# Optimization experiments

Measured on AMD Instinct MI355X. Metric: run time of the kernel, lower is better.

## Reference

```python
import jax, jax.numpy as jnp
import numpy as np

B, P, C = 256, 196, 512       # batch, num_pixels, encoder_dim
D, A, E = 512, 256, 256       # decoder_dim, attention_dim, embedding_dim
V, TC = 193, 256              # vocab, caption length (decode steps = TC-1)


def _lin(k, out_d, in_d):
    s = 1.0 / np.sqrt(in_d)
    return jax.random.uniform(k, (out_d, in_d), jnp.float32, -s, s)


def setup_inputs() -> dict:
    key = jax.random.key(0)
    ks = jax.random.split(key, 16)
    lens = jax.random.randint(ks[1], (B,), 2, TC + 1).at[0].set(TC)
    inp = {
        "encoder_output": jax.random.normal(ks[0], (B, P, C), jnp.float32),
        "encoded_captions": jax.random.randint(ks[2], (B, TC), 0, V),
        "caption_lengths": lens[:, None],
        # attention
        "W_enc_att": _lin(ks[3], A, C), "b_enc_att": jnp.zeros((A,), jnp.float32),
        "W_dec_att": _lin(ks[4], A, D), "b_dec_att": jnp.zeros((A,), jnp.float32),
        "W_full_att": _lin(ks[5], 1, A), "b_full_att": jnp.zeros((1,), jnp.float32),
        # embedding (init uniform(-0.1, 0.1) as in init_weigths)
        "embedding": jax.random.uniform(ks[6], (V, E), jnp.float32, -0.1, 0.1),
        # output projection
        "W_fc": jax.random.uniform(ks[7], (V, D), jnp.float32, -0.1, 0.1),
        "b_fc": jnp.zeros((V,), jnp.float32),
        # LSTMCell: input is [emb ; attended_enc] -> E + C
        "W_ih": _lin(ks[8], 4 * D, E + C), "b_ih": jnp.zeros((4 * D,), jnp.float32),
        "W_hh": _lin(ks[9], 4 * D, D), "b_hh": jnp.zeros((4 * D,), jnp.float32),
        # hidden/cell init + gate
        "W_init_h": _lin(ks[10], D, C), "b_init_h": jnp.zeros((D,), jnp.float32),
        "W_init_c": _lin(ks[11], D, C), "b_init_c": jnp.zeros((D,), jnp.float32),
        "W_fbeta": _lin(ks[12], D, C), "b_fbeta": jnp.zeros((D,), jnp.float32),
    }
    return inp


def reference(encoder_output, encoded_captions, caption_lengths,
              W_enc_att, b_enc_att, W_dec_att, b_dec_att, W_full_att, b_full_att,
              embedding, W_fc, b_fc, W_ih, b_ih, W_hh, b_hh,
              W_init_h, b_init_h, W_init_c, b_init_c, W_fbeta, b_fbeta):
    b = encoder_output.shape[0]
    enc = encoder_output.reshape(b, -1, encoder_output.shape[-1])  # [B,P,C]
    lens = caption_lengths[:, 0]
    sort_index = jnp.argsort(-lens)                 # descending length sort
    lens = lens[sort_index]
    enc = enc[sort_index]
    caps = encoded_captions[sort_index]
    decode_lengths = lens - 1
    T = caps.shape[1] - 1                           # static max decode steps

    embs = embedding[caps]                          # [B,TC,E]
    mean_enc = enc.mean(axis=1)                     # [B,C]
    h0 = mean_enc @ W_init_h.T + b_init_h
    c0 = mean_enc @ W_init_c.T + b_init_c

    enc_att = enc @ W_enc_att.T + b_enc_att         # [B,P,A] precomputed
    wf, bf = W_full_att[0], b_full_att[0]

    def step(carry, xs):
        h, c = carry
        emb_t, t = xs
        # soft attention
        dec_att = h @ W_dec_att.T + b_dec_att                       # [B,A]
        scores = jnp.einsum('bpa,a->bp',
                            jax.nn.relu(enc_att + dec_att[:, None, :]), wf) + bf
        alpha = jax.nn.softmax(scores, axis=1)                      # [B,P]
        awe = jnp.einsum('bpc,bp->bc', enc, alpha)                  # [B,C]
        gate = jax.nn.sigmoid(h @ W_fbeta.T + b_fbeta)              # [B,D]
        awe = gate * awe
        # LSTM cell (torch gate order: i,f,g,o); dropout is identity in eval
        x = jnp.concatenate([emb_t, awe], axis=1)                   # [B,E+C]
        gates = x @ W_ih.T + b_ih + h @ W_hh.T + b_hh
        i_g, f_g, g_g, o_g = jnp.split(gates, 4, axis=1)
        c_new = jax.nn.sigmoid(f_g) * c + jax.nn.sigmoid(i_g) * jnp.tanh(g_g)
        h_new = jax.nn.sigmoid(o_g) * jnp.tanh(c_new)
        # shrinking-batch semantics: inactive rows keep state, emit zeros
        active = (t < decode_lengths)[:, None]
        h2 = jnp.where(active, h_new, h)
        c2 = jnp.where(active, c_new, c)
        preds = jnp.where(active, h_new @ W_fc.T + b_fc, 0.0)
        alpha = jnp.where(active, alpha, 0.0)
        return (h2, c2), (preds, alpha)

    xs = (jnp.swapaxes(embs[:, :T], 0, 1), jnp.arange(T))
    _, (preds, alphas) = jax.lax.scan(step, (h0, c0), xs)
    predictions = jnp.swapaxes(preds, 0, 1)   # [B,T,V]
    alphas = jnp.swapaxes(alphas, 0, 1)       # [B,T,P]
    return predictions, caps, decode_lengths, alphas, sort_index
```

## Files before the change

### kernel.cpp

```cpp
#include <hip/hip_runtime.h>
#include <cstdint>
#include <cstddef>


typedef unsigned short u16;
typedef unsigned int u32;
typedef unsigned long long ull;
typedef __attribute__((ext_vector_type(8))) short short8;
typedef __attribute__((ext_vector_type(4))) float f32x4;

__device__ __forceinline__ float sigf(float x){ return 1.f/(1.f+expf(-x)); }
__device__ __forceinline__ u16 f2bf(float f){
  u32 u = __builtin_bit_cast(u32, f);
  u32 r = (u + 0x7fffu + ((u>>16)&1u)) >> 16;
  return (u16)r;
}
__device__ __forceinline__ float bf2f(u16 u){
  u32 x = ((u32)u) << 16;
  return __builtin_bit_cast(float, x);
}

__device__ __forceinline__ void st_dev_f32(float* p, float v){
  __hip_atomic_store(p, v, __ATOMIC_RELAXED, __HIP_MEMORY_SCOPE_AGENT);
}
__device__ __forceinline__ float ld_dev_f32(const float* p){
  return __hip_atomic_load(p, __ATOMIC_RELAXED, __HIP_MEMORY_SCOPE_AGENT);
}
__device__ __forceinline__ void st_dev_u16(u16* p, u16 v){
  __hip_atomic_store(p, v, __ATOMIC_RELAXED, __HIP_MEMORY_SCOPE_AGENT);
}
__device__ __forceinline__ void st_dev_u32(u32* p, u32 v){
  __hip_atomic_store(p, v, __ATOMIC_RELAXED, __HIP_MEMORY_SCOPE_AGENT);
}
__device__ __forceinline__ u32 ld_dev_u32(const u32* p){
  return __hip_atomic_load(p, __ATOMIC_RELAXED, __HIP_MEMORY_SCOPE_AGENT);
}
__device__ __forceinline__ ull ld_dev_u64(const ull* p){
  return __hip_atomic_load(p, __ATOMIC_RELAXED, __HIP_MEMORY_SCOPE_AGENT);
}

__device__ __forceinline__ void flag_store(int* f, int v){
  __syncthreads();
  if (threadIdx.x == 0)
    __hip_atomic_store(f, v, __ATOMIC_RELAXED, __HIP_MEMORY_SCOPE_AGENT);
}
__device__ __forceinline__ void flags_wait(const int* f, int n, int target){
  if (threadIdx.x < 64){
    const int lane = threadIdx.x;
    int spins = 0;
    for (;;){
      int v = (lane < n) ? __hip_atomic_load(&f[lane], __ATOMIC_RELAXED, __HIP_MEMORY_SCOPE_AGENT)
                         : 0x7fffffff;
      if (__all(v >= target)) break;
      if (++spins > (1<<20)) break;
      __builtin_amdgcn_s_sleep(2);
    }
  }
  __syncthreads();
}

__global__ void k_zero(float* a, int na4, float* b, int nb4, int* ctr){
  int i = blockIdx.x*blockDim.x + threadIdx.x;
  int stride = gridDim.x*blockDim.x;
  float4 z = make_float4(0.f,0.f,0.f,0.f);
  for (int j = i; j < na4; j += stride) ((float4*)a)[j] = z;
  for (int j = i; j < nb4; j += stride) ((float4*)b)[j] = z;
  if (i < 512) ctr[i] = 0;
}

__global__ void k_sort(const int* cap_lens, int* si, int* dlw, float* out_dl, float* out_si){
  __shared__ int lens[256];
  int tid = threadIdx.x;
  lens[tid] = cap_lens[tid];
  __syncthreads();
  int L = lens[tid];
  int rank = 0;
  for (int j = 0; j < 256; ++j){
    int Lj = lens[j];
    rank += ((Lj > L) || (Lj == L && j < tid)) ? 1 : 0;
  }
  si[rank] = tid;
  dlw[rank] = L - 1;
  out_dl[rank] = (float)(L - 1);
  out_si[rank] = (float)tid;
}

__global__ void k_caps(const int* caps, const int* si, int* caps_s, float* out_caps){
  int b = blockIdx.x, t = threadIdx.x;
  int v = caps[si[b]*256 + t];
  caps_s[b*256 + t] = v;
  out_caps[b*256 + t] = (float)v;
}

__global__ void k_prep(const float* enc, const int* si, u16* enc_sb){
  int b = blockIdx.x, tid = threadIdx.x;
  const float* src = enc + (size_t)si[b]*100352;
  u16* dst = enc_sb + (size_t)b*100352;
  for (int i = tid; i < 25088; i += 256){
    float4 v = *(const float4*)&src[i*4];
    ushort4 o;
    o.x = f2bf(v.x); o.y = f2bf(v.y); o.z = f2bf(v.z); o.w = f2bf(v.w);
    *(ushort4*)&dst[i*4] = o;
  }
}

__global__ void k_mean(const float* enc, const int* si, u16* mean_bf){
  int b = blockIdx.x, tid = threadIdx.x;
  const float* eb = enc + (size_t)si[b]*100352;
  int cc = 2*tid;
  float s0 = 0.f, s1 = 0.f;
  #pragma unroll 4
  for (int pp = 0; pp < 196; ++pp){
    float2 v = *(const float2*)&eb[(size_t)pp*512 + cc];
    s0 += v.x; s1 += v.y;
  }
  mean_bf[b*512 + cc]     = f2bf(s0 * (1.f/196.f));
  mean_bf[b*512 + cc + 1] = f2bf(s1 * (1.f/196.f));
}

struct ConcatP {
  const float *Wdec,*bdec,*Wfb,*bfb,*Wfc,*bfc,*Wih,*bih,*Whh,*bhh,*Winh,*binh,*Winc,*binc,*Wenc,*emb;
  u16 *Wc0,*Wc1,*Wc3,*Wenc_bf,*emb_bf;
  float *bc0,*bc1,*bc3;
};
__global__ void k_concat(ConcatP p){
  int idx = blockIdx.x*blockDim.x + threadIdx.x;
  int stride = gridDim.x*blockDim.x;
  for (int i = idx; i < 1024*512; i += stride){
    int n = i >> 9, k = i & 511;
    float v = (n < 512) ? p.Winh[n*512 + k] : p.Winc[(n-512)*512 + k];
    p.Wc0[i] = f2bf(v);
  }
  for (int i = idx; i < 1024; i += stride)
    p.bc0[i] = (i < 512) ? p.binh[i] : p.binc[i-512];
  for (int i = idx; i < 1024*512; i += stride){
    int n = i >> 9, k = i & 511;
    float v = (n < 256) ? p.Wdec[n*512+k]
            : (n < 768) ? p.Wfb[(n-256)*512+k]
            : (n < 961) ? p.Wfc[(n-768)*512+k] : 0.f;
    p.Wc1[i] = f2bf(v);
  }
  for (int i = idx; i < 1024; i += stride)
    p.bc1[i] = (i < 256) ? p.bdec[i] : (i < 768) ? p.bfb[i-256] : (i < 961) ? p.bfc[i-768] : 0.f;
  for (int i = idx; i < 2048*1280; i += stride){
    int n = i / 1280, k = i - n*1280;
    int j = n >> 2, g = n & 3, orow = g*512 + j;
    float v = (k < 768) ? p.Wih[orow*768 + k] : p.Whh[orow*512 + (k - 768)];
    p.Wc3[i] = f2bf(v);
  }
  for (int i = idx; i < 2048; i += stride){
    int j = i >> 2, g = i & 3, orow = g*512 + j;
    p.bc3[i] = p.bih[orow] + p.bhh[orow];
  }
  for (int i = idx; i < 256*512; i += stride) p.Wenc_bf[i] = f2bf(p.Wenc[i]);
  for (int i = idx; i < 193*256; i += stride) p.emb_bf[i] = f2bf(p.emb[i]);
}

struct MfmaP {
  const u16* A; const u16* Bw; const float* bias;
  int K, N;
  u16* out_bf;
  u16* h_bf; float* c;
};

template<int MODE, int NT>
__global__ __launch_bounds__(256) void k_mfma(MfmaP p){
  __shared__ __align__(16) unsigned char smem[16384 + 16384*NT];
  u16* As0 = (u16*)smem;
  u16* Bs0 = (u16*)(smem + 16384);

  const int tid  = threadIdx.x;
  const int bn0  = blockIdx.x * 64 * NT;
  const int bm0  = blockIdx.y * 64;
  const int wave = tid >> 6;
  const int lane = tid & 63;
  const int ln   = lane & 15;
  const int quad = lane >> 4;

  f32x4 acc[4][NT] = {};
  short8 pa[2], pb[2*NT];

  const int srow = tid >> 3;
  const int sgc  = tid & 7;

  #pragma unroll
  for (int r = 0; r < 2; ++r)
    pa[r] = *(const short8*)(p.A + (size_t)(bm0 + srow + 32*r)*p.K + sgc*8);
  #pragma unroll
  for (int r = 0; r < 2*NT; ++r)
    pb[r] = *(const short8*)(p.Bw + (size_t)(bn0 + srow + 32*r)*p.K + sgc*8);
  #pragma unroll
  for (int r = 0; r < 2; ++r){
    int row = srow + 32*r;
    *(short8*)&As0[row*64 + ((sgc ^ (row & 7))<<3)] = pa[r];
  }
  #pragma unroll
  for (int r = 0; r < 2*NT; ++r){
    int row = srow + 32*r;
    *(short8*)&Bs0[row*64 + ((sgc ^ (row & 7))<<3)] = pb[r];
  }

  const int nIter = p.K >> 6;
  int ib = 0;
  for (int it = 0; ; ){
    __syncthreads();
    const bool more = (it + 1 < nIter);
    if (more){
      int k0 = (it + 1) << 6;
      #pragma unroll
      for (int r = 0; r < 2; ++r)
        pa[r] = *(const short8*)(p.A + (size_t)(bm0 + srow + 32*r)*p.K + k0 + sgc*8);
      #pragma unroll
      for (int r = 0; r < 2*NT; ++r)
        pb[r] = *(const short8*)(p.Bw + (size_t)(bn0 + srow + 32*r)*p.K + k0 + sgc*8);
    }
    const u16* As = &As0[ib*4096];
    const u16* Bs = &Bs0[ib*4096*NT];
    #pragma unroll
    for (int kk = 0; kk < 2; ++kk){
      short8 af[4], bfr[NT];
      #pragma unroll
      for (int mt = 0; mt < 4; ++mt){
        int row = mt*16 + ln;
        int g = kk*4 + quad;
        af[mt] = *(const short8*)&As[row*64 + ((g ^ (row & 7))<<3)];
      }
      #pragma unroll
      for (int nt = 0; nt < NT; ++nt){
        int row = (wave*NT + nt)*16 + ln;
        int g = kk*4 + quad;
        bfr[nt] = *(const short8*)&Bs[row*64 + ((g ^ (row & 7))<<3)];
      }
      #pragma unroll
      for (int mt = 0; mt < 4; ++mt)
        #pragma unroll
        for (int nt = 0; nt < NT; ++nt)
          acc[mt][nt] = __builtin_amdgcn_mfma_f32_16x16x32_bf16(af[mt], bfr[nt], acc[mt][nt], 0, 0, 0);
    }
    if (!more) break;
    ib ^= 1;
    u16* Aw = &As0[ib*4096];
    u16* Bww = &Bs0[ib*4096*NT];
    #pragma unroll
    for (int r = 0; r < 2; ++r){
      int row = srow + 32*r;
      *(short8*)&Aw[row*64 + ((sgc ^ (row & 7))<<3)] = pa[r];
    }
    #pragma unroll
    for (int r = 0; r < 2*NT; ++r){
      int row = srow + 32*r;
      *(short8*)&Bww[row*64 + ((sgc ^ (row & 7))<<3)] = pb[r];
    }
    ++it;
  }

  #pragma unroll
  for (int nt = 0; nt < NT; ++nt){
    int n = bn0 + (wave*NT + nt)*16 + ln;
    float bv = p.bias[n];
    #pragma unroll
    for (int mt = 0; mt < 4; ++mt)
      #pragma unroll
      for (int r = 0; r < 4; ++r){
        int m = bm0 + mt*16 + quad*4 + r;
        float v = acc[mt][nt][r] + bv;
        if (MODE == 0){
          p.out_bf[(size_t)m*p.N + n] = f2bf(v);
        } else {
          if (n < 512) p.h_bf[m*512 + n] = f2bf(v);
          else         p.c[m*512 + n - 512] = v;
        }
      }
  }
}

struct PersistP {
  const u16* Wc1; const float* bc1;
  const u16* Wc3; const float* bc3;
  u16* h_bf; float* c; u16* z_bf;
  float* dec_att; float* gatev; float* preds; float* alphas;
  const u16* enc_att; const u16* enc_sb;
  const float* wfull; const float* bfull;
  const u16* emb_bf; const int* caps_s;
  const int* dl;
  int* ctr;
};

template<int NC, int MODE>
__device__ void gemm_phase(const PersistP& p, unsigned char* smem, int bm0, int bn0, int t){
  constexpr int K = NC * 64;
  constexpr int DP = (NC < 4) ? NC : 4;
  const u16* A    = (MODE == 2) ? p.h_bf : p.z_bf;
  const u16* Bw   = (MODE == 2) ? p.Wc1  : p.Wc3;
  const float* bias = (MODE == 2) ? p.bc1 : p.bc3;

  const int tid = threadIdx.x;
  const int w = tid >> 6, l = tid & 63;
  const int half = tid >> 9;
  const int loc = tid & 511;
  const int r = loc >> 3, g = loc & 7;
  u16* lds0 = (u16*)smem;
  u16* ldst = lds0 + (half ? 4096 : 0) + r*64 + ((g ^ (r & 7)) << 3);
  const u16* gp = half ? (Bw + (size_t)(bn0 + r)*K + g*8)
                       : (A  + (size_t)(bm0 + r)*K + g*8);
  const int mt = w >> 2, nt = w & 3;
  const int ln = l & 15, quad = l >> 4;
  f32x4 acc = {0.f,0.f,0.f,0.f};

  ull buf[DP][2];
  auto issue = [&](int ci, int slot){
    const u16* q = gp + ci*64;
    if (half == 0){
      buf[slot][0] = ld_dev_u64((const ull*)q);
      buf[slot][1] = ld_dev_u64((const ull*)q + 1);
    } else {
      buf[slot][0] = ((const ull*)q)[0];
      buf[slot][1] = ((const ull*)q)[1];
    }
  };
  auto wr = [&](int ci, int slot){
    u16* d = ldst + (ci & 1)*8192;
    ((ull*)d)[0] = buf[slot][0];
    ((ull*)d)[1] = buf[slot][1];
  };
  auto compute = [&](int ci){
    const u16* As = lds0 + (ci & 1)*8192;
    const u16* Bs = As + 4096;
    #pragma unroll
    for (int kk = 0; kk < 2; ++kk){
      int gg = kk*4 + quad;
      int ra = mt*16 + ln;
      short8 af = *(const short8*)&As[ra*64 + ((gg ^ (ra & 7))<<3)];
      int rb = nt*16 + ln;
      short8 bv = *(const short8*)&Bs[rb*64 + ((gg ^ (rb & 7))<<3)];
      acc = __builtin_amdgcn_mfma_f32_16x16x32_bf16(af, bv, acc, 0, 0, 0);
    }
  };

  #pragma unroll
  for (int s = 0; s < DP; ++s) issue(s, s);
  wr(0, 0);
  asm volatile("s_waitcnt lgkmcnt(0)" ::: "memory");
  __builtin_amdgcn_s_barrier();
  #pragma unroll
  for (int ci = 0; ci < NC; ++ci){
    if (ci + 1 < NC) wr(ci + 1, (ci + 1) % DP);
    if (ci + DP < NC) issue(ci + DP, (ci + DP) % DP);
    compute(ci);
    asm volatile("s_waitcnt lgkmcnt(0)" ::: "memory");
    __builtin_amdgcn_s_barrier();
  }

  if (MODE == 2){
    const int n = bn0 + nt*16 + ln;
    const float bv = bias[n];
    #pragma unroll
    for (int rr = 0; rr < 4; ++rr){
      int m = bm0 + mt*16 + quad*4 + rr;
      float v = acc[rr] + bv;
      if (n < 256)      st_dev_f32(&p.dec_att[m*256 + n], v);
      else if (n < 768) st_dev_f32(&p.gatev[m*512 + n - 256], sigf(v));
      else if (n < 961){
        int tp = t - 1;
        if (tp >= 0)
          p.preds[((size_t)m*255 + tp)*193 + (n - 768)] = (tp < p.dl[m]) ? v : 0.f;
      }
    }
  } else {
    float* Cs = (float*)smem;
    const int n_loc = nt*16 + ln;
    const float bv = bias[bn0 + n_loc];
    __syncthreads();
    #pragma unroll
    for (int rr = 0; rr < 4; ++rr)
      Cs[(mt*16 + quad*4 + rr)*68 + n_loc] = acc[rr] + bv;
    __syncthreads();
    {
      int m = tid >> 4, jl = tid & 15;
      float4 g4 = *(const float4*)&Cs[m*68 + jl*4];
      int gm = bm0 + m;
      int gj = (bn0 >> 2) + jl;
      if (t < p.dl[gm]){
        float ig = sigf(g4.x), fg = sigf(g4.y);
        float gg = tanhf(g4.z), og = sigf(g4.w);
        float cn = fg * p.c[gm*512 + gj] + ig * gg;
        float hn = og * tanhf(cn);
        p.c[gm*512 + gj] = cn;
        st_dev_u16(&p.h_bf[gm*512 + gj], f2bf(hn));
      }
    }
  }
}

__device__ void attn_phase(const PersistP& p, unsigned char* smem_raw, int b, int t,
                           const int* f_gate, int target){
  float* da  = (float*)smem_raw;
  float* wfs = da + 256;
  float* sc  = wfs + 256;
  float* awe = sc + 256;
  float* red = awe + 2048;
  const int tid = threadIdx.x;
  if (tid < 256){
    da[tid]  = ld_dev_f32(&p.dec_att[b*256 + tid]);
    wfs[tid] = p.wfull[tid];
  }
  __syncthreads();

  {
    const int pr = tid >> 2, aq = tid & 3;
    float s = 0.f;
    if (pr < 196){
      const u16* row = p.enc_att + ((size_t)b*196 + pr)*256 + aq*64;
      const float* dd = &da[aq*64];
      const float* ww = &wfs[aq*64];
      #pragma unroll
      for (int i = 0; i < 8; ++i){
        short8 v = *(const short8*)(row + i*8);
        #pragma unroll
        for (int j = 0; j < 8; ++j)
          s += fmaxf(bf2f((u16)v[j]) + dd[i*8+j], 0.f) * ww[i*8+j];
      }
    }
    s += __shfl_xor(s, 1, 64);
    s += __shfl_xor(s, 2, 64);
    if ((tid & 3) == 0 && pr < 196) sc[pr] = s + p.bfull[0];
  }
  __syncthreads();

  const int wid = tid >> 6, lane = tid & 63;
  float sv = (tid < 196) ? sc[tid] : -1e30f;
  float mx = sv;
  for (int o = 32; o > 0; o >>= 1) mx = fmaxf(mx, __shfl_down(mx, o, 64));
  if (lane == 0) red[wid] = mx;
  __syncthreads();
  if (tid == 0) red[16] = fmaxf(fmaxf(red[0], red[1]), fmaxf(red[2], red[3]));
  __syncthreads();
  mx = red[16];
  float e = (tid < 196) ? expf(sv - mx) : 0.f;
  float sm = e;
  for (int o = 32; o > 0; o >>= 1) sm += __shfl_down(sm, o, 64);
  if (lane == 0) red[wid] = sm;
  __syncthreads();
  if (tid == 0) red[16] = red[0] + red[1] + red[2] + red[3];
  __syncthreads();
  const float inv = 1.f / red[16];
  if (tid < 256) sc[tid] = e * inv;
  __syncthreads();
  if (tid < 196)
    p.alphas[((size_t)b*255 + t)*196 + tid] = sc[tid];

  {
    const int q = tid >> 8, cp = tid & 255, cc = 2*cp;
    const u16* eb = p.enc_sb + (size_t)b*100352;
    const int p0 = q*49;
    float v0 = 0.f, v1 = 0.f;
    #pragma unroll 7
    for (int i = 0; i < 49; ++i){
      int pp = p0 + i;
      u32 u = *(const u32*)&eb[(size_t)pp*512 + cc];
      float a = sc[pp];
      v0 += a * bf2f((u16)(u & 0xffffu));
      v1 += a * bf2f((u16)(u >> 16));
    }
    *(float2*)&awe[q*512 + cc] = make_float2(v0, v1);
  }

  flags_wait(f_gate, 8, target);

  if (tid < 256){
    const int cc = 2*tid;
    float v0 = awe[0*512+cc]   + awe[1*512+cc]   + awe[2*512+cc]   + awe[3*512+cc];
    float v1 = awe[0*512+cc+1] + awe[1*512+cc+1] + awe[2*512+cc+1] + awe[3*512+cc+1];
    u16* zb = p.z_bf + (size_t)b*1280;
    float g0 = ld_dev_f32(&p.gatev[b*512 + cc]);
    float g1 = ld_dev_f32(&p.gatev[b*512 + cc + 1]);
    st_dev_u16(&zb[256 + cc],     f2bf(g0 * v0));
    st_dev_u16(&zb[256 + cc + 1], f2bf(g1 * v1));
    int tok = p.caps_s[b*256 + t];
    st_dev_u16(&zb[tid], p.emb_bf[tok*256 + tid]);
    st_dev_u32((u32*)&zb[768 + cc], ld_dev_u32((const u32*)&p.h_bf[b*512 + cc]));
  }
}

__global__ __launch_bounds__(1024) void k_persist(PersistP p){
  __shared__ __align__(16) unsigned char smem[40960];
  const int b = blockIdx.x;
  int* f1 = p.ctr;
  int* f2 = p.ctr + 64;
  int* f3 = p.ctr + 320;
  for (int t = 0; t <= 255; ++t){
    if (b >= 192){
      const int idx = b - 192, x = idx & 15, y = idx >> 4;
      flags_wait(f3 + y*32, 32, t);
      if (p.dl[y*64] >= t)
        gemm_phase<8,2>(p, smem, y*64, x*64, t);
      flag_store(&f1[y*16 + x], t + 1);
    }
    if (t == 255) break;
    {
      const int y = b >> 6;
      if (t < p.dl[b]){
        flags_wait(f1 + y*16, 4, t + 1);
        attn_phase(p, smem, b, t, f1 + y*16 + 4, t + 1);
      }
      flag_store(&f2[b], t + 1);
    }
    if (b < 128){
      const int x = b & 31, y = b >> 5;
      flags_wait(f2 + y*64, 64, t + 1);
      if (p.dl[y*64] > t)
        gemm_phase<20,3>(p, smem, y*64, x*64, t);
      flag_store(&f3[y*32 + x], t + 1);
    }
  }
}

extern "C" void kernel_launch(void* const* d_in, const int* in_sizes, int n_in,
                              void* d_out, int out_size, void* d_ws, size_t ws_size,
                              hipStream_t stream){
  (void)in_sizes; (void)n_in; (void)out_size; (void)ws_size;
  const float* enc   = (const float*)d_in[0];
  const int*   caps  = (const int*)d_in[1];
  const int*   clens = (const int*)d_in[2];
  const float* Wenc  = (const float*)d_in[3];
  const float* benc  = (const float*)d_in[4];
  const float* Wdec  = (const float*)d_in[5];
  const float* bdec  = (const float*)d_in[6];
  const float* Wfull = (const float*)d_in[7];
  const float* bfull = (const float*)d_in[8];
  const float* emb   = (const float*)d_in[9];
  const float* Wfc   = (const float*)d_in[10];
  const float* bfc   = (const float*)d_in[11];
  const float* Wih   = (const float*)d_in[12];
  const float* bih   = (const float*)d_in[13];
  const float* Whh   = (const float*)d_in[14];
  const float* bhh   = (const float*)d_in[15];
  const float* Winh  = (const float*)d_in[16];
  const float* binh  = (const float*)d_in[17];
  const float* Winc  = (const float*)d_in[18];
  const float* binc  = (const float*)d_in[19];
  const float* Wfb   = (const float*)d_in[20];
  const float* bfb   = (const float*)d_in[21];

  float* out       = (float*)d_out;
  float* out_preds = out;
  float* out_caps  = out + 12599040;
  float* out_dl    = out + 12664576;
  float* out_alph  = out + 12664832;
  float* out_si    = out + 25459712;

  char* w = (char*)d_ws;
  size_t off = 0;
  auto alloc = [&](size_t bytes) -> void* {
    void* pp = w + off; off += (bytes + 255) & ~(size_t)255; return pp;
  };
  int*   si      = (int*)  alloc(256*4);
  int*   dlw     = (int*)  alloc(256*4);
  int*   caps_s  = (int*)  alloc(65536*4);
  float* c       = (float*)alloc(131072*4);
  float* dec_att = (float*)alloc(65536*4);
  float* gatev   = (float*)alloc(131072*4);
  float* bc0     = (float*)alloc(1024*4);
  float* bc1     = (float*)alloc(1024*4);
  float* bc3     = (float*)alloc(2048*4);
  int*   ctr     = (int*)  alloc(1024*4);
  u16*   mean_bf = (u16*)  alloc(131072*2);
  u16*   h_bf    = (u16*)  alloc(131072*2);
  u16*   z_bf    = (u16*)  alloc(327680*2);
  u16*   Wc0     = (u16*)  alloc(524288*2);
  u16*   Wc1     = (u16*)  alloc(524288*2);
  u16*   Wc3     = (u16*)  alloc(2621440*2);
  u16*   Wenc_bf = (u16*)  alloc(131072*2);
  u16*   emb_bf  = (u16*)  alloc(49408*2);
  u16*   enc_sb  = (u16*)  alloc(25690112ull*2);
  u16*   enc_att = (u16*)  alloc(12845056ull*2);

  k_zero<<<1024, 256, 0, stream>>>(out_preds, 12599040/4, out_alph, 12794880/4, ctr);
  k_sort<<<1, 256, 0, stream>>>(clens, si, dlw, out_dl, out_si);
  k_caps<<<256, 256, 0, stream>>>(caps, si, caps_s, out_caps);
  k_prep<<<256, 256, 0, stream>>>(enc, si, enc_sb);
  k_mean<<<256, 256, 0, stream>>>(enc, si, mean_bf);
  ConcatP cp{Wdec,bdec,Wfb,bfb,Wfc,bfc,Wih,bih,Whh,bhh,Winh,binh,Winc,binc,Wenc,emb,
             Wc0,Wc1,Wc3,Wenc_bf,emb_bf,bc0,bc1,bc3};
  k_concat<<<2048, 256, 0, stream>>>(cp);

  {
    MfmaP g{};
    g.A = mean_bf; g.Bw = Wc0; g.bias = bc0; g.K = 512; g.N = 1024;
    g.h_bf = h_bf; g.c = c;
    k_mfma<1,1><<<dim3(16,4), 256, 0, stream>>>(g);
  }
  {
    MfmaP g{};
    g.A = enc_sb; g.Bw = Wenc_bf; g.bias = benc; g.K = 512; g.N = 256;
    g.out_bf = enc_att;
    k_mfma<0,2><<<dim3(2,784), 256, 0, stream>>>(g);
  }

  PersistP pp{};
  pp.Wc1 = Wc1; pp.bc1 = bc1; pp.Wc3 = Wc3; pp.bc3 = bc3;
  pp.h_bf = h_bf; pp.c = c; pp.z_bf = z_bf;
  pp.dec_att = dec_att; pp.gatev = gatev; pp.preds = out_preds; pp.alphas = out_alph;
  pp.enc_att = enc_att; pp.enc_sb = enc_sb;
  pp.wfull = Wfull; pp.bfull = bfull;
  pp.emb_bf = emb_bf; pp.caps_s = caps_s;
  pp.dl = dlw; pp.ctr = ctr;

  void* kargs[] = { (void*)&pp };
  hipError_t e = hipLaunchCooperativeKernel((const void*)k_persist, dim3(256), dim3(1024),
                                            kargs, 0, stream);
  if (e != hipSuccess){
    k_persist<<<dim3(256), dim3(1024), 0, stream>>>(pp);
  }
}
```

Baseline: 8.167 ms.

## Deepen GEMM global-load pipeline with raw dwordx4 loads and 4-stage LDS ring

Restructures the persistent kernel's GEMM phase so that global loads are issued as inline-asm dwordx4 loads, with sc1 on the activation half to keep coherence, and a prefetch depth of 6. Explicit vmcnt waits replace compiler-scheduled waits, and LDS is used as a 4-slot ring with one barrier per chunk. Dynamic shared memory is raised to 96KB to hold the ring. A redundant __syncthreads in the LSTM epilogue is dropped and the flag-polling sleep is shortened. The larger LDS footprint and manual waitcnt handling risk ordering bugs and rely on one 1024-thread block per CU still fitting.

```diff
diff --git a/kernel.cpp b/kernel.cpp
--- a/kernel.cpp
+++ b/kernel.cpp
@@ -35,8 +35,16 @@
 __device__ __forceinline__ u32 ld_dev_u32(const u32* p){
   return __hip_atomic_load(p, __ATOMIC_RELAXED, __HIP_MEMORY_SCOPE_AGENT);
 }
-__device__ __forceinline__ ull ld_dev_u64(const ull* p){
-  return __hip_atomic_load(p, __ATOMIC_RELAXED, __HIP_MEMORY_SCOPE_AGENT);
+
+__device__ __forceinline__ void wait_vm1(int ahead){
+  switch(ahead){
+    case 5: asm volatile("s_waitcnt vmcnt(5)" ::: "memory"); break;
+    case 4: asm volatile("s_waitcnt vmcnt(4)" ::: "memory"); break;
+    case 3: asm volatile("s_waitcnt vmcnt(3)" ::: "memory"); break;
+    case 2: asm volatile("s_waitcnt vmcnt(2)" ::: "memory"); break;
+    case 1: asm volatile("s_waitcnt vmcnt(1)" ::: "memory"); break;
+    default: asm volatile("s_waitcnt vmcnt(0)" ::: "memory"); break;
+  }
 }
 
 __device__ __forceinline__ void flag_store(int* f, int v){
@@ -53,7 +61,7 @@
                          : 0x7fffffff;
       if (__all(v >= target)) break;
       if (++spins > (1<<20)) break;
-      __builtin_amdgcn_s_sleep(2);
+      __builtin_amdgcn_s_sleep(1);
     }
   }
   __syncthreads();
@@ -268,7 +276,7 @@
           p.out_bf[(size_t)m*p.N + n] = f2bf(v);
         } else {
           if (n < 512) p.h_bf[m*512 + n] = f2bf(v);
-          else         p.c[m*512 + n - 512] = v;
+        else         p.c[m*512 + n - 512] = v;
         }
       }
   }
@@ -289,7 +297,7 @@
 template<int NC, int MODE>
 __device__ void gemm_phase(const PersistP& p, unsigned char* smem, int bm0, int bn0, int t){
   constexpr int K = NC * 64;
-  constexpr int DP = (NC < 4) ? NC : 4;
+  constexpr int DP = (NC < 6) ? NC : 6;
   const u16* A    = (MODE == 2) ? p.h_bf : p.z_bf;
   const u16* Bw   = (MODE == 2) ? p.Wc1  : p.Wc3;
   const float* bias = (MODE == 2) ? p.bc1 : p.bc3;
@@ -307,24 +315,19 @@
   const int ln = l & 15, quad = l >> 4;
   f32x4 acc = {0.f,0.f,0.f,0.f};
 
-  ull buf[DP][2];
+  f32x4 buf[6];
   auto issue = [&](int ci, int slot){
-    const u16* q = gp + ci*64;
-    if (half == 0){
-      buf[slot][0] = ld_dev_u64((const ull*)q);
-      buf[slot][1] = ld_dev_u64((const ull*)q + 1);
-    } else {
-      buf[slot][0] = ((const ull*)q)[0];
-      buf[slot][1] = ((const ull*)q)[1];
-    }
+    const void* q = gp + ci*64;
+    if (half == 0)
+      asm volatile("global_load_dwordx4 %0, %1, off sc1" : "=&v"(buf[slot]) : "v"(q));
+    else
+      asm volatile("global_load_dwordx4 %0, %1, off"     : "=&v"(buf[slot]) : "v"(q));
   };
   auto wr = [&](int ci, int slot){
-    u16* d = ldst + (ci & 1)*8192;
-    ((ull*)d)[0] = buf[slot][0];
-    ((ull*)d)[1] = buf[slot][1];
+    *(f32x4*)(ldst + (ci & 3)*8192) = buf[slot];
   };
   auto compute = [&](int ci){
-    const u16* As = lds0 + (ci & 1)*8192;
+    const u16* As = lds0 + (ci & 3)*8192;
     const u16* Bs = As + 4096;
     #pragma unroll
     for (int kk = 0; kk < 2; ++kk){
@@ -337,19 +340,22 @@
     }
   };
 
+  asm volatile("s_waitcnt vmcnt(0)" ::: "memory");
   #pragma unroll
   for (int s = 0; s < DP; ++s) issue(s, s);
-  wr(0, 0);
+  #pragma unroll
+  for (int ci = 0; ci < NC; ++ci){
+    wait_vm1(((ci + DP < NC) ? DP : (NC - ci)) - 1);
+    __builtin_amdgcn_sched_barrier(0);
+    wr(ci, ci % DP);
+    asm volatile("s_waitcnt lgkmcnt(0)" ::: "memory");
+    __builtin_amdgcn_s_barrier();
+    __builtin_amdgcn_sched_barrier(0);
+    if (ci + DP < NC) issue(ci + DP, ci % DP);
+    compute(ci);
+  }
   asm volatile("s_waitcnt lgkmcnt(0)" ::: "memory");
   __builtin_amdgcn_s_barrier();
-  #pragma unroll
-  for (int ci = 0; ci < NC; ++ci){
-    if (ci + 1 < NC) wr(ci + 1, (ci + 1) % DP);
-    if (ci + DP < NC) issue(ci + DP, (ci + DP) % DP);
-    compute(ci);
-    asm volatile("s_waitcnt lgkmcnt(0)" ::: "memory");
-    __builtin_amdgcn_s_barrier();
-  }
 
   if (MODE == 2){
     const int n = bn0 + nt*16 + ln;
@@ -370,7 +376,6 @@
     float* Cs = (float*)smem;
     const int n_loc = nt*16 + ln;
     const float bv = bias[bn0 + n_loc];
-    __syncthreads();
     #pragma unroll
     for (int rr = 0; rr < 4; ++rr)
       Cs[(mt*16 + quad*4 + rr)*68 + n_loc] = acc[rr] + bv;
@@ -483,7 +488,7 @@
 }
 
 __global__ __launch_bounds__(1024) void k_persist(PersistP p){
-  __shared__ __align__(16) unsigned char smem[40960];
+  extern __shared__ __align__(16) unsigned char smem[];
   const int b = blockIdx.x;
   int* f1 = p.ctr;
   int* f2 = p.ctr + 64;
@@ -606,10 +611,14 @@
   pp.emb_bf = emb_bf; pp.caps_s = caps_s;
   pp.dl = dlw; pp.ctr = ctr;
 
+  const int shmem = 98304;
+  hipFuncSetAttribute((const void*)k_persist,
+                      hipFuncAttributeMaxDynamicSharedMemorySize, shmem);
+
   void* kargs[] = { (void*)&pp };
   hipError_t e = hipLaunchCooperativeKernel((const void*)k_persist, dim3(256), dim3(1024),
-                                            kargs, 0, stream);
+                                            kargs, shmem, stream);
   if (e != hipSuccess){
-    k_persist<<<dim3(256), dim3(1024), 0, stream>>>(pp);
-  }
-}
+    k_persist<<<dim3(256), dim3(1024), shmem, stream>>>(pp);
+  }
+}
```

Result: slower. 10.87 ms (+33.1%).

## Replace persistent cooperative kernel with per-timestep launches of specialized blocks

Applied to the files above, without the earlier changes.

The single persistent cooperative kernel, which looped over all timesteps with flag-based inter-block syncs, becomes 256 launches of a per-step kernel. Each launch runs 448 blocks: 64 for the decoder-projection GEMM, 256 for attention and 128 for the LSTM GEMM. Kernel boundaries now order work across timesteps, so the cross-step f3 flags go away and the GEMM and h_bf writes can use plain loads and stores instead of agent-scope atomics. Flag waits remain only within a step and spin with a shorter sleep. This trades the persistent kernel's spin-wait overhead for 256 kernel-launch overheads, and it depends on the three block roles being co-resident so the in-step flag waits cannot deadlock.

```diff
diff --git a/kernel.cpp b/kernel.cpp
--- a/kernel.cpp
+++ b/kernel.cpp
@@ -31,9 +31,6 @@
 }
 __device__ __forceinline__ void st_dev_u32(u32* p, u32 v){
   __hip_atomic_store(p, v, __ATOMIC_RELAXED, __HIP_MEMORY_SCOPE_AGENT);
-}
-__device__ __forceinline__ u32 ld_dev_u32(const u32* p){
-  return __hip_atomic_load(p, __ATOMIC_RELAXED, __HIP_MEMORY_SCOPE_AGENT);
 }
 __device__ __forceinline__ ull ld_dev_u64(const ull* p){
   return __hip_atomic_load(p, __ATOMIC_RELAXED, __HIP_MEMORY_SCOPE_AGENT);
@@ -53,7 +50,7 @@
                          : 0x7fffffff;
       if (__all(v >= target)) break;
       if (++spins > (1<<20)) break;
-      __builtin_amdgcn_s_sleep(2);
+      __builtin_amdgcn_s_sleep(1);
     }
   }
   __syncthreads();
@@ -274,7 +271,7 @@
   }
 }
 
-struct PersistP {
+struct StepP {
   const u16* Wc1; const float* bc1;
   const u16* Wc3; const float* bc3;
   u16* h_bf; float* c; u16* z_bf;
@@ -284,10 +281,11 @@
   const u16* emb_bf; const int* caps_s;
   const int* dl;
   int* ctr;
+  int t;
 };
 
-template<int NC, int MODE>
-__device__ void gemm_phase(const PersistP& p, unsigned char* smem, int bm0, int bn0, int t){
+template<int NC, int MODE, bool COH>
+__device__ void gemm_phase(const StepP& p, unsigned char* smem, int bm0, int bn0, int t){
   constexpr int K = NC * 64;
   constexpr int DP = (NC < 4) ? NC : 4;
   const u16* A    = (MODE == 2) ? p.h_bf : p.z_bf;
@@ -310,7 +308,7 @@
   ull buf[DP][2];
   auto issue = [&](int ci, int slot){
     const u16* q = gp + ci*64;
-    if (half == 0){
+    if (COH && half == 0){
       buf[slot][0] = ld_dev_u64((const ull*)q);
       buf[slot][1] = ld_dev_u64((const ull*)q + 1);
     } else {
@@ -370,7 +368,6 @@
     float* Cs = (float*)smem;
     const int n_loc = nt*16 + ln;
     const float bv = bias[bn0 + n_loc];
-    __syncthreads();
     #pragma unroll
     for (int rr = 0; rr < 4; ++rr)
       Cs[(mt*16 + quad*4 + rr)*68 + n_loc] = acc[rr] + bv;
@@ -386,13 +383,13 @@
         float cn = fg * p.c[gm*512 + gj] + ig * gg;
         float hn = og * tanhf(cn);
         p.c[gm*512 + gj] = cn;
-        st_dev_u16(&p.h_bf[gm*512 + gj], f2bf(hn));
+        p.h_bf[gm*512 + gj] = f2bf(hn);
       }
     }
   }
 }
 
-__device__ void attn_phase(const PersistP& p, unsigned char* smem_raw, int b, int t,
+__device__ void attn_phase(const StepP& p, unsigned char* smem_raw, int b, int t,
                            const int* f_gate, int target){
   float* da  = (float*)smem_raw;
   float* wfs = da + 256;
@@ -478,39 +475,34 @@
     st_dev_u16(&zb[256 + cc + 1], f2bf(g1 * v1));
     int tok = p.caps_s[b*256 + t];
     st_dev_u16(&zb[tid], p.emb_bf[tok*256 + tid]);
-    st_dev_u32((u32*)&zb[768 + cc], ld_dev_u32((const u32*)&p.h_bf[b*512 + cc]));
-  }
-}
-
-__global__ __launch_bounds__(1024) void k_persist(PersistP p){
+    st_dev_u32((u32*)&zb[768 + cc], *(const u32*)&p.h_bf[b*512 + cc]);
+  }
+}
+
+__global__ __launch_bounds__(1024) void k_step(StepP p){
   __shared__ __align__(16) unsigned char smem[40960];
   const int b = blockIdx.x;
+  const int t = p.t;
   int* f1 = p.ctr;
   int* f2 = p.ctr + 64;
-  int* f3 = p.ctr + 320;
-  for (int t = 0; t <= 255; ++t){
-    if (b >= 192){
-      const int idx = b - 192, x = idx & 15, y = idx >> 4;
-      flags_wait(f3 + y*32, 32, t);
-      if (p.dl[y*64] >= t)
-        gemm_phase<8,2>(p, smem, y*64, x*64, t);
-      flag_store(&f1[y*16 + x], t + 1);
-    }
-    if (t == 255) break;
-    {
-      const int y = b >> 6;
-      if (t < p.dl[b]){
-        flags_wait(f1 + y*16, 4, t + 1);
-        attn_phase(p, smem, b, t, f1 + y*16 + 4, t + 1);
-      }
-      flag_store(&f2[b], t + 1);
-    }
-    if (b < 128){
-      const int x = b & 31, y = b >> 5;
+  if (b < 64){
+    const int x = b & 15, y = b >> 4;
+    if (p.dl[y*64] >= t)
+      gemm_phase<8,2,false>(p, smem, y*64, x*64, t);
+    flag_store(&f1[y*16 + x], t + 1);
+  } else if (b < 320){
+    const int bb = b - 64;
+    const int y = bb >> 6;
+    if (t < p.dl[bb]){
+      flags_wait(f1 + y*16, 4, t + 1);
+      attn_phase(p, smem, bb, t, f1 + y*16 + 4, t + 1);
+    }
+    flag_store(&f2[bb], t + 1);
+  } else {
+    const int idx = b - 320, x = idx & 31, y = idx >> 5;
+    if (p.dl[y*64] > t){
       flags_wait(f2 + y*64, 64, t + 1);
-      if (p.dl[y*64] > t)
-        gemm_phase<20,3>(p, smem, y*64, x*64, t);
-      flag_store(&f3[y*32 + x], t + 1);
+      gemm_phase<20,3,true>(p, smem, y*64, x*64, t);
     }
   }
 }
@@ -597,19 +589,17 @@
     k_mfma<0,2><<<dim3(2,784), 256, 0, stream>>>(g);
   }
 
-  PersistP pp{};
-  pp.Wc1 = Wc1; pp.bc1 = bc1; pp.Wc3 = Wc3; pp.bc3 = bc3;
-  pp.h_bf = h_bf; pp.c = c; pp.z_bf = z_bf;
-  pp.dec_att = dec_att; pp.gatev = gatev; pp.preds = out_preds; pp.alphas = out_alph;
-  pp.enc_att = enc_att; pp.enc_sb = enc_sb;
-  pp.wfull = Wfull; pp.bfull = bfull;
-  pp.emb_bf = emb_bf; pp.caps_s = caps_s;
-  pp.dl = dlw; pp.ctr = ctr;
-
-  void* kargs[] = { (void*)&pp };
-  hipError_t e = hipLaunchCooperativeKernel((const void*)k_persist, dim3(256), dim3(1024),
-                                            kargs, 0, stream);
-  if (e != hipSuccess){
-    k_persist<<<dim3(256), dim3(1024), 0, stream>>>(pp);
-  }
-}
+  StepP sp{};
+  sp.Wc1 = Wc1; sp.bc1 = bc1; sp.Wc3 = Wc3; sp.bc3 = bc3;
+  sp.h_bf = h_bf; sp.c = c; sp.z_bf = z_bf;
+  sp.dec_att = dec_att; sp.gatev = gatev; sp.preds = out_preds; sp.alphas = out_alph;
+  sp.enc_att = enc_att; sp.enc_sb = enc_sb;
+  sp.wfull = Wfull; sp.bfull = bfull;
+  sp.emb_bf = emb_bf; sp.caps_s = caps_s;
+  sp.dl = dlw; sp.ctr = ctr;
+
+  for (int t = 0; t <= 255; ++t){
+    sp.t = t;
+    k_step<<<448, 1024, 0, stream>>>(sp);
+  }
+}
```

Measured after the change: 7.556 ms. -7.5%, faster.
